# Kernel optimization log

Hardware: AMD Instinct MI355X
Metric: run time of the kernel (lower is better)

## Reference

```python
import jax, jax.numpy as jnp
import numpy as np

WINDOW = 127          # odd
W = (WINDOW - 1) // 2 # 63 half-window
Q_CH = WINDOW + 1     # 128 query chunk
K_CH = WINDOW * 2     # 254 key chunk


def _compl_mod(m, n):
    return int(n * int(np.ceil(m / n)) - m)


def setup_inputs() -> dict:
    key = jax.random.key(0)
    kq, kk, kv = jax.random.split(key, 3)
    B, L, NH, H = 4, 4096, 16, 64
    return {
        "q": jax.random.normal(kq, (B, L, NH, H), dtype=jnp.float32),
        "k": jax.random.normal(kk, (B, L, NH, H), dtype=jnp.float32),
        "v": jax.random.normal(kv, (B, L, NH, H), dtype=jnp.float32),
    }


def _build_mask(c, k_pad, dtype_bool=bool):
    # base band mask over one (q_ch, k_ch) block: True = masked out
    u = jnp.triu(jnp.ones((Q_CH, K_CH), dtype=bool))
    band = jnp.logical_and(u, jnp.flip(u, (0, 1)))
    base = ~band
    mask_left = base.at[:, :W].set(True)
    mask_right = base.at[:, K_CH - (W + k_pad):].set(True)
    if c > 1:
        mid = jnp.broadcast_to(base, (c - 2, Q_CH, K_CH)) if c > 2 else jnp.zeros((0, Q_CH, K_CH), bool)
        return jnp.concatenate([mask_left[None], mid, mask_right[None]], axis=0)
    return jnp.logical_or(mask_left, mask_right)[None]


def reference(q, k, v):
    b, s, nh, h = q.shape
    q = q * (h ** -0.5)

    q_pad = _compl_mod(s, Q_CH)
    k_pad = _compl_mod(s + 2 * W - K_CH, Q_CH)

    # chunk queries: (b, c, q_ch, nh, h)
    qp = jnp.pad(q, ((0, 0), (0, q_pad), (0, 0), (0, 0)))
    c = (s + q_pad) // Q_CH
    qw = qp.reshape(b, c, Q_CH, nh, h)

    # overlapping key/value windows via gather: (b, c, k_ch, nh, h)
    kp = jnp.pad(k, ((0, 0), (W, W + k_pad), (0, 0), (0, 0)))
    vp = jnp.pad(v, ((0, 0), (W, W + k_pad), (0, 0), (0, 0)))
    starts = np.arange(c) * Q_CH
    idx = starts[:, None] + np.arange(K_CH)[None, :]  # (c, k_ch)
    kw = kp[:, idx]
    vw = vp[:, idx]

    # block scores: (b, nh, c, q_ch, k_ch)
    A = jnp.einsum('bcqnh,bcknh->bncqk', qw, kw)

    mask = _build_mask(c, k_pad)  # (c, q_ch, k_ch)
    neg = -jnp.finfo(A.dtype).max
    A = jnp.where(mask[None, None], neg, A)
    A = jax.nn.softmax(A, axis=-1)

    z = jnp.einsum('bncqk,bcknh->bncqh', A, vw)  # (b, nh, c, q_ch, h)
    z = z.reshape(b, nh, c * Q_CH, h)[:, :, :s]
    return jnp.transpose(z, (0, 2, 1, 3))  # (b, s, nh, h)
```

## Files before the change

### kernel.cpp

```cpp
#include <hip/hip_runtime.h>


typedef _Float16 f16;
typedef _Float16 f16x2  __attribute__((ext_vector_type(2)));
typedef _Float16 f16x4  __attribute__((ext_vector_type(4)));
typedef _Float16 f16x8  __attribute__((ext_vector_type(8)));
typedef float    f32x16 __attribute__((ext_vector_type(16)));
typedef int      int4v  __attribute__((ext_vector_type(4)));

constexpr int NB = 4, L = 4096, NH = 16, H = 64;
constexpr int CQ = 128, NC = L / CQ, KW = 256, WR = 63;
constexpr int RS = NH * H;

constexpr int Q_OFF = 0;
constexpr int K_OFF = 16384;
constexpr int V_OFF = 49152;
constexpr int LDS_BYTES = 81920;

#define DEV static __device__ __forceinline__

DEV int iclamp(int x, int lo, int hi) { return x < lo ? lo : (x > hi ? hi : x); }

DEV float fexp2(float x) {
#if __has_builtin(__builtin_amdgcn_exp2f)
    return __builtin_amdgcn_exp2f(x);
#else
    return exp2f(x);
#endif
}

DEV int packh2(float a, float b) {
    f16x2 p; p.x = (f16)a; p.y = (f16)b;
    return __builtin_bit_cast(int, p);
}

DEV int rmaddr(int row, int colb) {
    return row * 128 + (colb ^ ((row & 7) << 4));
}

DEV int vaddr(int h, int kb) {
    return (h * 512 + kb) ^ ((((h & 7) ^ ((h >> 3) & 7))) << 4);
}

DEV int oaddr(int row, int col) {
    return (row * 64 + col) ^ ((row & 3) << 2);
}

DEV void swap_halves(int& a, int& b, int hi) {
    int pa = __shfl_xor(a, 32, 64);
    int pb = __shfl_xor(b, 32, 64);
    int na = hi ? pb : a;
    int nb = hi ? b  : pa;
    a = na; b = nb;
}

__global__ __launch_bounds__(256) __attribute__((amdgpu_waves_per_eu(2, 2)))
void wattn_kernel(const float* __restrict__ q_, const float* __restrict__ k_,
                  const float* __restrict__ v_, float* __restrict__ o_)
{
    __shared__ alignas(16) char smem[LDS_BYTES];
    char*  Q_lds = smem + Q_OFF;
    char*  K_lds = smem + K_OFF;
    char*  V_lds = smem + V_OFF;
    float* O_lds = (float*)smem;

    const int bid = (int)blockIdx.x;
    const int wid = (bid & 7) * ((NB * NH * NC) / 8) + (bid >> 3);
    const int c = wid & (NC - 1);
    const int n = (wid >> 5) & (NH - 1);
    const int b = wid >> 9;

    const int t    = (int)threadIdx.x;
    const int lane = t & 63;
    const int wq   = t >> 6;
    const int lq   = lane & 31;
    const int hi   = lane >> 5;

    const int kg0 = c * CQ - WR;
    const size_t bn = ((size_t)b * L * NH + n) * H;
    const float qs = 0.125f * 1.44269504088896f;

    const int rr = t >> 4;
    const int h4 = (t & 15) << 2;
    const int cb = h4 << 1;

    {
        const float* qp = q_ + bn + (size_t)(c * CQ) * RS + h4;
        #pragma unroll
        for (int p = 0; p < 8; ++p) {
            int r = rr + p * 16;
            float4 x = *(const float4*)(qp + (size_t)r * RS);
            *(f16x4*)(Q_lds + rmaddr(r, cb)) =
                (f16x4){(f16)(x.x * qs), (f16)(x.y * qs), (f16)(x.z * qs), (f16)(x.w * qs)};
        }
    }
    {
        #pragma unroll
        for (int p = 0; p < 16; ++p) {
            int r  = rr + p * 16;
            int kr = iclamp(kg0 + r, 0, L - 1);
            float4 x = *(const float4*)(k_ + bn + (size_t)kr * RS + h4);
            *(f16x4*)(K_lds + rmaddr(r, cb)) =
                (f16x4){(f16)x.x, (f16)x.y, (f16)x.z, (f16)x.w};
        }
    }
    {
        const int r0_ = (t >> 4) << 1;
        #pragma unroll
        for (int p = 0; p < 8; ++p) {
            int r0  = r0_ + p * 32;
            int kr0 = iclamp(kg0 + r0,     0, L - 1);
            int kr1 = iclamp(kg0 + r0 + 1, 0, L - 1);
            float4 v0 = *(const float4*)(v_ + bn + (size_t)kr0 * RS + h4);
            float4 v1 = *(const float4*)(v_ + bn + (size_t)kr1 * RS + h4);
            *(f16x2*)(V_lds + vaddr(h4 + 0, r0 * 2)) = (f16x2){(f16)v0.x, (f16)v1.x};
            *(f16x2*)(V_lds + vaddr(h4 + 1, r0 * 2)) = (f16x2){(f16)v0.y, (f16)v1.y};
            *(f16x2*)(V_lds + vaddr(h4 + 2, r0 * 2)) = (f16x2){(f16)v0.z, (f16)v1.z};
            *(f16x2*)(V_lds + vaddr(h4 + 3, r0 * 2)) = (f16x2){(f16)v0.w, (f16)v1.w};
        }
    }

    const int iq  = wq * 32 + lq;
    const int jlo = (c == 0) ? WR : 0;
    const int jhi = (KW < L - kg0) ? KW : (L - kg0);
    const int lo  = (iq > jlo) ? iq : jlo;
    const int hb  = (iq + 126 < jhi - 1) ? (iq + 126) : (jhi - 1);
    const unsigned span = (unsigned)(hb - lo);

    f32x16 o0, o1;
    #pragma unroll
    for (int r = 0; r < 16; ++r) { o0[r] = 0.f; o1[r] = 0.f; }
    float dsum = 0.f;

    __syncthreads();

    f16x8 qf[4];
    {
        const int qrow = wq * 32 + lq;
        #pragma unroll
        for (int tq = 0; tq < 4; ++tq)
            qf[tq] = *(const f16x8*)(Q_lds + rmaddr(qrow, 32 * tq + 16 * hi));
    }

    #pragma unroll
    for (int i = 0; i < 5; ++i) {
        const int kt = wq + i;
        const int krow = kt * 32 + lq;
        f16x8 kf[4];
        #pragma unroll
        for (int tq = 0; tq < 4; ++tq)
            kf[tq] = *(const f16x8*)(K_lds + rmaddr(krow, 32 * tq + 16 * hi));

        f32x16 s;
        #pragma unroll
        for (int r = 0; r < 16; ++r) s[r] = 0.f;
        #pragma unroll
        for (int tq = 0; tq < 4; ++tq)
            s = __builtin_amdgcn_mfma_f32_32x32x16_f16(kf[tq], qf[tq], s, 0, 0, 0);

        const int jb = kt * 32 + 4 * hi;
        float pe[16];
        #pragma unroll
        for (int r = 0; r < 16; ++r) {
            int j = jb + (r & 3) + ((r >> 2) << 3);
            float e = fexp2(s[r]);
            e = ((unsigned)(j - lo) <= span) ? e : 0.f;
            dsum += e;
            pe[r] = e;
        }
        int d0 = packh2(pe[0],  pe[1]),  d1 = packh2(pe[2],  pe[3]);
        int d2 = packh2(pe[4],  pe[5]),  d3 = packh2(pe[6],  pe[7]);
        int d4 = packh2(pe[8],  pe[9]),  d5 = packh2(pe[10], pe[11]);
        int d6 = packh2(pe[12], pe[13]), d7 = packh2(pe[14], pe[15]);
        swap_halves(d0, d2, hi); swap_halves(d1, d3, hi);
        swap_halves(d4, d6, hi); swap_halves(d5, d7, hi);
        f16x8 pa0 = __builtin_bit_cast(f16x8, (int4v){d0, d1, d2, d3});
        f16x8 pa1 = __builtin_bit_cast(f16x8, (int4v){d4, d5, d6, d7});

        const int kb = kt * 64 + hi * 16;
        f16x8 vb00 = *(const f16x8*)(V_lds + vaddr(lq,      kb));
        f16x8 vb01 = *(const f16x8*)(V_lds + vaddr(lq,      kb + 32));
        f16x8 vb10 = *(const f16x8*)(V_lds + vaddr(32 + lq, kb));
        f16x8 vb11 = *(const f16x8*)(V_lds + vaddr(32 + lq, kb + 32));
        o0 = __builtin_amdgcn_mfma_f32_32x32x16_f16(pa0, vb00, o0, 0, 0, 0);
        o0 = __builtin_amdgcn_mfma_f32_32x32x16_f16(pa1, vb01, o0, 0, 0, 0);
        o1 = __builtin_amdgcn_mfma_f32_32x32x16_f16(pa0, vb10, o1, 0, 0, 0);
        o1 = __builtin_amdgcn_mfma_f32_32x32x16_f16(pa1, vb11, o1, 0, 0, 0);
    }

    float dtot = dsum + __shfl_xor(dsum, 32, 64);
    float dinv = 1.0f / dtot;

    __syncthreads();

    #pragma unroll
    for (int r = 0; r < 16; ++r) {
        int qloc = (r & 3) + ((r >> 2) << 3) + 4 * hi;
        float rd = __shfl(dinv, qloc, 64);
        int row = wq * 32 + qloc;
        O_lds[oaddr(row, lq)]      = o0[r] * rd;
        O_lds[oaddr(row, 32 + lq)] = o1[r] * rd;
    }
    __syncthreads();

    const size_t ob = ((size_t)b * L + (size_t)c * CQ) * RS + (size_t)n * H;
    #pragma unroll
    for (int it = 0; it < 8; ++it) {
        int flat = it * 256 + t;
        int row  = flat >> 4;
        int hh   = (flat & 15) << 2;
        float4 val = *(const float4*)(O_lds + oaddr(row, hh));
        *(float4*)(o_ + ob + (size_t)row * RS + hh) = val;
    }
}

extern "C" void kernel_launch(void* const* d_in, const int* in_sizes, int n_in,
                              void* d_out, int out_size, void* d_ws, size_t ws_size,
                              hipStream_t stream) {
    const float* q = (const float*)d_in[0];
    const float* k = (const float*)d_in[1];
    const float* v = (const float*)d_in[2];
    float* o = (float*)d_out;
    (void)in_sizes; (void)n_in; (void)out_size; (void)d_ws; (void)ws_size;
    wattn_kernel<<<dim3(NB * NH * NC), dim3(256), 0, stream>>>(q, k, v, o);
}
```

Baseline: 54.42 us.

## Split key tiles across two wave halves with LDS reduction of partial outputs

Block size doubles to 512 threads. The 5 key tiles per query tile are split between two wave groups (3 and 2 tiles), and the partial output accumulators and softmax denominators are combined through LDS before normalization. The intent is to shorten the serial MFMA/exp chain per wave and give each CU more waves to hide memory latency while loading inputs. The cost is an extra LDS round trip, an added barrier, unequal work between the two halves, and possibly more register or occupancy pressure under the new launch bounds.

```diff
diff --git a/kernel.cpp b/kernel.cpp
--- a/kernel.cpp
+++ b/kernel.cpp
@@ -34,12 +34,12 @@
     return __builtin_bit_cast(int, p);
 }
 
-DEV int rmaddr(int row, int colb) {
-    return row * 128 + (colb ^ ((row & 7) << 4));
+DEV int rmaddr(int base, int r, int colb) {
+    return base + r * 128 + (colb ^ ((r & 7) << 4));
 }
 
 DEV int vaddr(int h, int kb) {
-    return (h * 512 + kb) ^ ((((h & 7) ^ ((h >> 3) & 7))) << 4);
+    return V_OFF + ((h * 512 + kb) ^ ((((h & 7) ^ ((h >> 3) & 7))) << 4));
 }
 
 DEV int oaddr(int row, int col) {
@@ -54,15 +54,13 @@
     a = na; b = nb;
 }
 
-__global__ __launch_bounds__(256) __attribute__((amdgpu_waves_per_eu(2, 2)))
+__global__ __launch_bounds__(512, 4)
 void wattn_kernel(const float* __restrict__ q_, const float* __restrict__ k_,
                   const float* __restrict__ v_, float* __restrict__ o_)
 {
     __shared__ alignas(16) char smem[LDS_BYTES];
-    char*  Q_lds = smem + Q_OFF;
-    char*  K_lds = smem + K_OFF;
-    char*  V_lds = smem + V_OFF;
     float* O_lds = (float*)smem;
+    float* D_lds = (float*)(smem + 32768);
 
     const int bid = (int)blockIdx.x;
     const int wid = (bid & 7) * ((NB * NH * NC) / 8) + (bid >> 3);
@@ -72,55 +70,53 @@
 
     const int t    = (int)threadIdx.x;
     const int lane = t & 63;
-    const int wq   = t >> 6;
+    const int w    = t >> 6;
     const int lq   = lane & 31;
     const int hi   = lane >> 5;
+    const int qt   = w & 3;
+    const int half = w >> 2;
 
     const int kg0 = c * CQ - WR;
     const size_t bn = ((size_t)b * L * NH + n) * H;
     const float qs = 0.125f * 1.44269504088896f;
 
-    const int rr = t >> 4;
     const int h4 = (t & 15) << 2;
     const int cb = h4 << 1;
+    const int ru = t >> 4;
 
     {
         const float* qp = q_ + bn + (size_t)(c * CQ) * RS + h4;
         #pragma unroll
-        for (int p = 0; p < 8; ++p) {
-            int r = rr + p * 16;
+        for (int p = 0; p < 4; ++p) {
+            int r = ru + p * 32;
             float4 x = *(const float4*)(qp + (size_t)r * RS);
-            *(f16x4*)(Q_lds + rmaddr(r, cb)) =
+            *(f16x4*)(smem + rmaddr(Q_OFF, r, cb)) =
                 (f16x4){(f16)(x.x * qs), (f16)(x.y * qs), (f16)(x.z * qs), (f16)(x.w * qs)};
         }
     }
-    {
-        #pragma unroll
-        for (int p = 0; p < 16; ++p) {
-            int r  = rr + p * 16;
-            int kr = iclamp(kg0 + r, 0, L - 1);
-            float4 x = *(const float4*)(k_ + bn + (size_t)kr * RS + h4);
-            *(f16x4*)(K_lds + rmaddr(r, cb)) =
-                (f16x4){(f16)x.x, (f16)x.y, (f16)x.z, (f16)x.w};
-        }
-    }
-    {
-        const int r0_ = (t >> 4) << 1;
-        #pragma unroll
-        for (int p = 0; p < 8; ++p) {
-            int r0  = r0_ + p * 32;
-            int kr0 = iclamp(kg0 + r0,     0, L - 1);
-            int kr1 = iclamp(kg0 + r0 + 1, 0, L - 1);
-            float4 v0 = *(const float4*)(v_ + bn + (size_t)kr0 * RS + h4);
-            float4 v1 = *(const float4*)(v_ + bn + (size_t)kr1 * RS + h4);
-            *(f16x2*)(V_lds + vaddr(h4 + 0, r0 * 2)) = (f16x2){(f16)v0.x, (f16)v1.x};
-            *(f16x2*)(V_lds + vaddr(h4 + 1, r0 * 2)) = (f16x2){(f16)v0.y, (f16)v1.y};
-            *(f16x2*)(V_lds + vaddr(h4 + 2, r0 * 2)) = (f16x2){(f16)v0.z, (f16)v1.z};
-            *(f16x2*)(V_lds + vaddr(h4 + 3, r0 * 2)) = (f16x2){(f16)v0.w, (f16)v1.w};
-        }
-    }
-
-    const int iq  = wq * 32 + lq;
+    #pragma unroll
+    for (int p = 0; p < 8; ++p) {
+        int r  = ru + p * 32;
+        int kr = iclamp(kg0 + r, 0, L - 1);
+        float4 x = *(const float4*)(k_ + bn + (size_t)kr * RS + h4);
+        *(f16x4*)(smem + rmaddr(K_OFF, r, cb)) =
+            (f16x4){(f16)x.x, (f16)x.y, (f16)x.z, (f16)x.w};
+    }
+    #pragma unroll
+    for (int p = 0; p < 4; ++p) {
+        int r0  = ru * 2 + p * 64;
+        int kr0 = iclamp(kg0 + r0,     0, L - 1);
+        int kr1 = iclamp(kg0 + r0 + 1, 0, L - 1);
+        float4 v0 = *(const float4*)(v_ + bn + (size_t)kr0 * RS + h4);
+        float4 v1 = *(const float4*)(v_ + bn + (size_t)kr1 * RS + h4);
+        int kb = r0 * 2;
+        *(f16x2*)(smem + vaddr(h4 + 0, kb)) = (f16x2){(f16)v0.x, (f16)v1.x};
+        *(f16x2*)(smem + vaddr(h4 + 1, kb)) = (f16x2){(f16)v0.y, (f16)v1.y};
+        *(f16x2*)(smem + vaddr(h4 + 2, kb)) = (f16x2){(f16)v0.z, (f16)v1.z};
+        *(f16x2*)(smem + vaddr(h4 + 3, kb)) = (f16x2){(f16)v0.w, (f16)v1.w};
+    }
+
+    const int iq  = qt * 32 + lq;
     const int jlo = (c == 0) ? WR : 0;
     const int jhi = (KW < L - kg0) ? KW : (L - kg0);
     const int lo  = (iq > jlo) ? iq : jlo;
@@ -135,21 +131,15 @@
     __syncthreads();
 
     f16x8 qf[4];
-    {
-        const int qrow = wq * 32 + lq;
+    #pragma unroll
+    for (int tq = 0; tq < 4; ++tq)
+        qf[tq] = *(const f16x8*)(smem + rmaddr(Q_OFF, qt * 32 + lq, 32 * tq + 16 * hi));
+
+    auto body = [&](int kt) {
+        f16x8 kf[4];
         #pragma unroll
         for (int tq = 0; tq < 4; ++tq)
-            qf[tq] = *(const f16x8*)(Q_lds + rmaddr(qrow, 32 * tq + 16 * hi));
-    }
-
-    #pragma unroll
-    for (int i = 0; i < 5; ++i) {
-        const int kt = wq + i;
-        const int krow = kt * 32 + lq;
-        f16x8 kf[4];
-        #pragma unroll
-        for (int tq = 0; tq < 4; ++tq)
-            kf[tq] = *(const f16x8*)(K_lds + rmaddr(krow, 32 * tq + 16 * hi));
+            kf[tq] = *(const f16x8*)(smem + rmaddr(K_OFF, kt * 32 + lq, 32 * tq + 16 * hi));
 
         f32x16 s;
         #pragma unroll
@@ -178,35 +168,55 @@
         f16x8 pa1 = __builtin_bit_cast(f16x8, (int4v){d4, d5, d6, d7});
 
         const int kb = kt * 64 + hi * 16;
-        f16x8 vb00 = *(const f16x8*)(V_lds + vaddr(lq,      kb));
-        f16x8 vb01 = *(const f16x8*)(V_lds + vaddr(lq,      kb + 32));
-        f16x8 vb10 = *(const f16x8*)(V_lds + vaddr(32 + lq, kb));
-        f16x8 vb11 = *(const f16x8*)(V_lds + vaddr(32 + lq, kb + 32));
+        f16x8 vb00 = *(const f16x8*)(smem + vaddr(lq,      kb));
+        f16x8 vb01 = *(const f16x8*)(smem + vaddr(lq,      kb + 32));
+        f16x8 vb10 = *(const f16x8*)(smem + vaddr(32 + lq, kb));
+        f16x8 vb11 = *(const f16x8*)(smem + vaddr(32 + lq, kb + 32));
         o0 = __builtin_amdgcn_mfma_f32_32x32x16_f16(pa0, vb00, o0, 0, 0, 0);
         o0 = __builtin_amdgcn_mfma_f32_32x32x16_f16(pa1, vb01, o0, 0, 0, 0);
         o1 = __builtin_amdgcn_mfma_f32_32x32x16_f16(pa0, vb10, o1, 0, 0, 0);
         o1 = __builtin_amdgcn_mfma_f32_32x32x16_f16(pa1, vb11, o1, 0, 0, 0);
-    }
-
-    float dtot = dsum + __shfl_xor(dsum, 32, 64);
-    float dinv = 1.0f / dtot;
-
-    __syncthreads();
-
-    #pragma unroll
-    for (int r = 0; r < 16; ++r) {
-        int qloc = (r & 3) + ((r >> 2) << 3) + 4 * hi;
-        float rd = __shfl(dinv, qloc, 64);
-        int row = wq * 32 + qloc;
-        O_lds[oaddr(row, lq)]      = o0[r] * rd;
-        O_lds[oaddr(row, 32 + lq)] = o1[r] * rd;
+    };
+
+    const int kt0 = qt + half * 3;
+    body(kt0);
+    body(kt0 + 1);
+    if (!half) body(kt0 + 2);
+
+    float dw = dsum + __shfl_xor(dsum, 32, 64);
+
+    __syncthreads();
+
+    if (half) {
+        #pragma unroll
+        for (int r = 0; r < 16; ++r) {
+            int qloc = (r & 3) + ((r >> 2) << 3) + 4 * hi;
+            int row  = qt * 32 + qloc;
+            O_lds[oaddr(row, lq)]      = o0[r];
+            O_lds[oaddr(row, 32 + lq)] = o1[r];
+        }
+        if (lane < 32) D_lds[qt * 32 + lq] = dw;
+    }
+    __syncthreads();
+
+    if (!half) {
+        float dinv = 1.0f / (dw + D_lds[iq]);
+        #pragma unroll
+        for (int r = 0; r < 16; ++r) {
+            int qloc = (r & 3) + ((r >> 2) << 3) + 4 * hi;
+            int row  = qt * 32 + qloc;
+            float rd = __shfl(dinv, qloc, 64);
+            int a0 = oaddr(row, lq), a1 = oaddr(row, 32 + lq);
+            O_lds[a0] = (o0[r] + O_lds[a0]) * rd;
+            O_lds[a1] = (o1[r] + O_lds[a1]) * rd;
+        }
     }
     __syncthreads();
 
     const size_t ob = ((size_t)b * L + (size_t)c * CQ) * RS + (size_t)n * H;
     #pragma unroll
-    for (int it = 0; it < 8; ++it) {
-        int flat = it * 256 + t;
+    for (int it = 0; it < 4; ++it) {
+        int flat = it * 512 + t;
         int row  = flat >> 4;
         int hh   = (flat & 15) << 2;
         float4 val = *(const float4*)(O_lds + oaddr(row, hh));
@@ -222,5 +232,5 @@
     const float* v = (const float*)d_in[2];
     float* o = (float*)d_out;
     (void)in_sizes; (void)n_in; (void)out_size; (void)d_ws; (void)ws_size;
-    wattn_kernel<<<dim3(NB * NH * NC), dim3(256), 0, stream>>>(q, k, v, o);
-}
+    wattn_kernel<<<dim3(NB * NH * NC), dim3(512), 0, stream>>>(q, k, v, o);
+}
```

Result: faster. 49.92 us (-8.3%).
